# Kernel tuning notes

Measured on AMD Instinct MI355X. Metric: run time of the kernel, lower is better.

## Reference

```python
import jax, jax.numpy as jnp
import numpy as np
from jax import lax

N, C_IN, L = 32, 256, 4096
C_OUT, K, GROUPS = 256, 9, 4
C_DIM, PAD, STRIDE = 128, 4, 1


def setup_inputs() -> dict:
    key = jax.random.key(0)
    k1, k2, k3, k4, k5 = jax.random.split(key, 5)
    x = jax.random.normal(k1, (N, C_IN, L), dtype=jnp.float32)
    c = jax.random.normal(k2, (N, C_DIM), dtype=jnp.float32)
    weight = jax.random.normal(k3, (C_OUT, C_IN // GROUPS, K), dtype=jnp.float32)
    c_weight = jax.random.normal(k4, (C_OUT, C_DIM), dtype=jnp.float32)
    bias = jax.random.normal(k5, (C_OUT,), dtype=jnp.float32)
    return {"x": x, "c": c, "weight": weight, "c_weight": c_weight, "bias": bias}


def reference(x, c, weight, c_weight, bias):
    # Grouped conv1d: equivalent to the unfold+per-group matmul in the torch code.
    # dims: x (N, C_in, L), weight (C_out, C_in/groups, K) -> out (N, C_out, L_out)
    out = lax.conv_general_dilated(
        x, weight,
        window_strides=(STRIDE,),
        padding=[(PAD, PAD)],
        dimension_numbers=("NCH", "OIH", "NCH"),
        feature_group_count=GROUPS,
    )
    # Concat-path context: cat([patches, c]) @ cat([W, cW]).T == conv(x) + c @ cW.T,
    # with the context term broadcast over all temporal positions.
    ctx = jnp.einsum("nd,od->no", c, c_weight)  # (N, C_out)
    out = out + ctx[:, :, None] + bias[None, :, None]
    return out
```

## Files before the change

kernel.cpp:

```cpp
#include <hip/hip_runtime.h>
#include <hip/hip_bf16.h>

#define NB     32
#define CIN    256
#define LIN    4096
#define COUT   256
#define KW     9
#define NGRP   4
#define CDIM   128
#define CPG    64
#define LT     256
#define NROWS  264
#define RP     68
#define WF_ELEMS (4*4*9*2*64*8)

typedef __attribute__((ext_vector_type(8))) short short8;
typedef __attribute__((ext_vector_type(4))) short short4v;
typedef __attribute__((ext_vector_type(4))) float float4v;
typedef __attribute__((ext_vector_type(4))) unsigned short ushort4v;

__global__ void pack_weights(const float* __restrict__ w, __hip_bfloat16* __restrict__ wF) {
    int tid = blockIdx.x * blockDim.x + threadIdx.x;
    if (tid >= WF_ELEMS) return;
    int j    = tid & 7;
    int lane = (tid >> 3) & 63;
    int rest = tid >> 9;
    int chunk = rest & 1;  rest >>= 1;
    int k     = rest % 9;  rest /= 9;
    int co16  = rest & 3;
    int g     = rest >> 2;
    int co = g * CPG + co16 * 16 + (lane & 15);
    int ci = chunk * 32 + (lane >> 4) * 8 + j;
    wF[tid] = __float2bfloat16(w[(co * CPG + ci) * KW + k]);
}

__global__ __launch_bounds__(256) void ctx_kernel(const float* __restrict__ c,
                                                  const float* __restrict__ cw,
                                                  const float* __restrict__ bias,
                                                  float* __restrict__ ctxb) {
    int gw   = (blockIdx.x * 256 + threadIdx.x) >> 6;
    int lane = threadIdx.x & 63;
    int n  = gw >> 8;
    int co = gw & 255;
    float s = c[n * CDIM + lane]      * cw[co * CDIM + lane]
            + c[n * CDIM + 64 + lane] * cw[co * CDIM + 64 + lane];
    #pragma unroll
    for (int off = 32; off; off >>= 1) s += __shfl_down(s, off);
    if (lane == 0) ctxb[gw] = s + bias[co];
}

__global__ __launch_bounds__(256, 4) void conv_mfma(
    const float* __restrict__ x, const __hip_bfloat16* __restrict__ wF,
    const float* __restrict__ ctxb, float* __restrict__ out)
{
    __shared__ unsigned short sx[NROWS * RP];
    __shared__ float sctx[CPG];

    const int bx = blockIdx.x;
    const int t  = bx & 15;
    const int g  = (bx >> 4) & 3;
    const int n  = bx >> 6;
    const int l0 = t * LT;
    const int tid = threadIdx.x;
    const int lane = tid & 63;
    const int wv   = tid >> 6;

    if (tid < CPG) sctx[tid] = ctxb[n * COUT + g * CPG + tid];

    const float* xb = x + ((size_t)(n * CIN + g * CPG)) * LIN;

    {
        int q4  = 1 + (lane & 15);
        int cqb = 4 * wv + (lane >> 4);
        #pragma unroll
        for (int i = 0; i < 4; ++i, q4 += 16) {
            int lg = l0 - 4 + 4 * q4;
            float4v v[4];
            #pragma unroll
            for (int j = 0; j < 4; ++j)
                v[j] = *(const float4v*)(xb + (size_t)(4 * cqb + j) * LIN + lg);
            int row = 4 * q4;
            #pragma unroll
            for (int d = 0; d < 4; ++d) {
                ushort4v p;
                #pragma unroll
                for (int j = 0; j < 4; ++j)
                    p[j] = __builtin_bit_cast(unsigned short, __float2bfloat16(v[j][d]));
                *(ushort4v*)(&sx[(row + d) * RP + 4 * cqb]) = p;
            }
        }
    }
    if (tid < 32) {
        int head = (tid < 16);
        int q4 = head ? 0 : 65;
        int cq = tid & 15;
        int lg = l0 - 4 + 4 * q4;
        bool ok = head ? (t > 0) : (t < 15);
        float4v v[4];
        #pragma unroll
        for (int j = 0; j < 4; ++j)
            v[j] = ok ? *(const float4v*)(xb + (size_t)(4 * cq + j) * LIN + lg)
                      : (float4v){0.f, 0.f, 0.f, 0.f};
        int row = 4 * q4;
        #pragma unroll
        for (int d = 0; d < 4; ++d) {
            ushort4v p;
            #pragma unroll
            for (int j = 0; j < 4; ++j)
                p[j] = __builtin_bit_cast(unsigned short, __float2bfloat16(v[j][d]));
            *(ushort4v*)(&sx[(row + d) * RP + 4 * cq]) = p;
        }
    }
    __syncthreads();

    const int r  = lane & 15;
    const int q  = lane >> 4;
    const int wl = wv * 64;

    float4v acc[4][4];
    #pragma unroll
    for (int a = 0; a < 4; ++a)
        #pragma unroll
        for (int b = 0; b < 4; ++b)
            acc[a][b] = (float4v){0.f, 0.f, 0.f, 0.f};

    const short8* wFp = (const short8*)wF;

    #pragma unroll
    for (int k = 0; k < KW; ++k) {
        #pragma unroll
        for (int chunk = 0; chunk < 2; ++chunk) {
            short8 bfrag[4];
            #pragma unroll
            for (int l16 = 0; l16 < 4; ++l16) {
                int row = wl + l16 * 16 + r + k;
                int base = row * RP + chunk * 32 + q * 8;
                short4v lo = *(const short4v*)(&sx[base]);
                short4v hi = *(const short4v*)(&sx[base + 4]);
                bfrag[l16] = __builtin_shufflevector(lo, hi, 0, 1, 2, 3, 4, 5, 6, 7);
            }
            short8 afrag[4];
            #pragma unroll
            for (int co16 = 0; co16 < 4; ++co16) {
                afrag[co16] = wFp[(((g * 4 + co16) * 9 + k) * 2 + chunk) * 64 + lane];
            }
            #pragma unroll
            for (int co16 = 0; co16 < 4; ++co16)
                #pragma unroll
                for (int l16 = 0; l16 < 4; ++l16)
                    acc[co16][l16] = __builtin_amdgcn_mfma_f32_16x16x32_bf16(
                        afrag[co16], bfrag[l16], acc[co16][l16], 0, 0, 0);
        }
    }

    float* ob = out + ((size_t)(n * COUT + g * CPG)) * LIN + l0 + wl;
    #pragma unroll
    for (int co16 = 0; co16 < 4; ++co16) {
        #pragma unroll
        for (int reg = 0; reg < 4; ++reg) {
            int co_l = co16 * 16 + q * 4 + reg;
            float add = sctx[co_l];
            #pragma unroll
            for (int l16 = 0; l16 < 4; ++l16) {
                ob[(size_t)co_l * LIN + l16 * 16 + r] = acc[co16][l16][reg] + add;
            }
        }
    }
}

extern "C" void kernel_launch(void* const* d_in, const int* in_sizes, int n_in,
                              void* d_out, int out_size, void* d_ws, size_t ws_size,
                              hipStream_t stream) {
    const float* x    = (const float*)d_in[0];
    const float* c    = (const float*)d_in[1];
    const float* w    = (const float*)d_in[2];
    const float* cw   = (const float*)d_in[3];
    const float* bias = (const float*)d_in[4];
    float* out = (float*)d_out;

    __hip_bfloat16* wF = (__hip_bfloat16*)d_ws;
    float* ctxb = (float*)((char*)d_ws + (size_t)WF_ELEMS * 2);

    pack_weights<<<(WF_ELEMS + 255) / 256, 256, 0, stream>>>(w, wF);
    ctx_kernel<<<(NB * COUT * 64) / 256, 256, 0, stream>>>(c, cw, bias, ctxb);
    conv_mfma<<<NB * NGRP * (LIN / LT), 256, 0, stream>>>(x, wF, ctxb, out);
}
```

Measured before the change: 259.9 us.

## Loop each block over four L tiles with double-buffered LDS prefetch

Each block now walks four consecutive 128-wide L tiles instead of computing one 256-wide tile. While the MFMAs run on the current LDS buffer, the next tile's x data and halo are loaded into registers, then converted to bf16 and written into a second LDS buffer. The four waves are rearranged as a 2x2 split over L and output channels, so each wave holds half as many accumulators. The aim is to hide global load latency behind compute, at the cost of twice the LDS footprint and a smaller grid.

```diff
diff --git a/kernel.cpp b/kernel.cpp
--- a/kernel.cpp
+++ b/kernel.cpp
@@ -9,9 +9,11 @@
 #define NGRP   4
 #define CDIM   128
 #define CPG    64
-#define LT     256
-#define NROWS  264
+#define LT     128
+#define NROWS  136
 #define RP     68
+#define TPB    4
+#define NTILES 32
 #define WF_ELEMS (4*4*9*2*64*8)
 
 typedef __attribute__((ext_vector_type(8))) short short8;
@@ -53,15 +55,14 @@
     const float* __restrict__ x, const __hip_bfloat16* __restrict__ wF,
     const float* __restrict__ ctxb, float* __restrict__ out)
 {
-    __shared__ unsigned short sx[NROWS * RP];
+    __shared__ unsigned short sx[2][NROWS * RP];
     __shared__ float sctx[CPG];
 
     const int bx = blockIdx.x;
-    const int t  = bx & 15;
-    const int g  = (bx >> 4) & 3;
-    const int n  = bx >> 6;
-    const int l0 = t * LT;
-    const int tid = threadIdx.x;
+    const int tb = bx & 7;
+    const int g  = (bx >> 3) & 3;
+    const int n  = bx >> 5;
+    const int tid  = threadIdx.x;
     const int lane = tid & 63;
     const int wv   = tid >> 6;
 
@@ -69,102 +70,132 @@
 
     const float* xb = x + ((size_t)(n * CIN + g * CPG)) * LIN;
 
-    {
-        int q4  = 1 + (lane & 15);
-        int cqb = 4 * wv + (lane >> 4);
-        #pragma unroll
-        for (int i = 0; i < 4; ++i, q4 += 16) {
-            int lg = l0 - 4 + 4 * q4;
-            float4v v[4];
+    const int cqb = 4 * wv + (lane >> 4);
+    const int q4a = 1 + (lane & 15);
+
+    float4v mv[8];
+    float4v hv[2];
+
+    auto issue_main = [&](int l0) {
+        #pragma unroll
+        for (int i = 0; i < 2; ++i) {
+            int lg = l0 - 4 + 4 * (q4a + 16 * i);
             #pragma unroll
             for (int j = 0; j < 4; ++j)
-                v[j] = *(const float4v*)(xb + (size_t)(4 * cqb + j) * LIN + lg);
-            int row = 4 * q4;
+                mv[4 * i + j] = *(const float4v*)(xb + (size_t)(4 * cqb + j) * LIN + lg);
+        }
+    };
+    auto issue_halo = [&](int gt, int l0) {
+        if (tid < 64) {
+            int side = tid >> 5;
+            bool ok  = side ? (gt < NTILES - 1) : (gt > 0);
+            int lg   = side ? (l0 + LT) : (l0 - 4);
+            int cr   = 4 * ((tid >> 1) & 15) + 2 * (tid & 1);
+            #pragma unroll
+            for (int j = 0; j < 2; ++j)
+                hv[j] = ok ? *(const float4v*)(xb + (size_t)(cr + j) * LIN + lg)
+                           : (float4v){0.f, 0.f, 0.f, 0.f};
+        }
+    };
+    auto write_tile = [&](unsigned short* s) {
+        #pragma unroll
+        for (int i = 0; i < 2; ++i) {
+            int row0 = 4 * (q4a + 16 * i);
             #pragma unroll
             for (int d = 0; d < 4; ++d) {
                 ushort4v p;
                 #pragma unroll
                 for (int j = 0; j < 4; ++j)
-                    p[j] = __builtin_bit_cast(unsigned short, __float2bfloat16(v[j][d]));
-                *(ushort4v*)(&sx[(row + d) * RP + 4 * cqb]) = p;
-            }
-        }
-    }
-    if (tid < 32) {
-        int head = (tid < 16);
-        int q4 = head ? 0 : 65;
-        int cq = tid & 15;
-        int lg = l0 - 4 + 4 * q4;
-        bool ok = head ? (t > 0) : (t < 15);
-        float4v v[4];
-        #pragma unroll
-        for (int j = 0; j < 4; ++j)
-            v[j] = ok ? *(const float4v*)(xb + (size_t)(4 * cq + j) * LIN + lg)
-                      : (float4v){0.f, 0.f, 0.f, 0.f};
-        int row = 4 * q4;
-        #pragma unroll
-        for (int d = 0; d < 4; ++d) {
-            ushort4v p;
-            #pragma unroll
-            for (int j = 0; j < 4; ++j)
-                p[j] = __builtin_bit_cast(unsigned short, __float2bfloat16(v[j][d]));
-            *(ushort4v*)(&sx[(row + d) * RP + 4 * cq]) = p;
-        }
-    }
-    __syncthreads();
+                    p[j] = __builtin_bit_cast(unsigned short, __float2bfloat16(mv[4 * i + j][d]));
+                *(ushort4v*)(&s[(row0 + d) * RP + 4 * cqb]) = p;
+            }
+        }
+        if (tid < 64) {
+            int side = tid >> 5;
+            int row0 = side ? (NROWS - 4) : 0;
+            int off  = 4 * ((tid >> 1) & 15) + 2 * (tid & 1);
+            #pragma unroll
+            for (int d = 0; d < 4; ++d) {
+                unsigned int pp =
+                    (unsigned int)__builtin_bit_cast(unsigned short, __float2bfloat16(hv[0][d]))
+                  | ((unsigned int)__builtin_bit_cast(unsigned short, __float2bfloat16(hv[1][d])) << 16);
+                *(unsigned int*)(&s[(row0 + d) * RP + off]) = pp;
+            }
+        }
+    };
 
     const int r  = lane & 15;
     const int q  = lane >> 4;
-    const int wl = wv * 64;
-
-    float4v acc[4][4];
-    #pragma unroll
-    for (int a = 0; a < 4; ++a)
-        #pragma unroll
-        for (int b = 0; b < 4; ++b)
-            acc[a][b] = (float4v){0.f, 0.f, 0.f, 0.f};
+    const int wl = (wv >> 1) * 64;
+    const int wc = (wv & 1) * 32;
+    const int c0 = (wv & 1) * 2;
 
     const short8* wFp = (const short8*)wF;
-
-    #pragma unroll
-    for (int k = 0; k < KW; ++k) {
-        #pragma unroll
-        for (int chunk = 0; chunk < 2; ++chunk) {
-            short8 bfrag[4];
-            #pragma unroll
-            for (int l16 = 0; l16 < 4; ++l16) {
-                int row = wl + l16 * 16 + r + k;
-                int base = row * RP + chunk * 32 + q * 8;
-                short4v lo = *(const short4v*)(&sx[base]);
-                short4v hi = *(const short4v*)(&sx[base + 4]);
-                bfrag[l16] = __builtin_shufflevector(lo, hi, 0, 1, 2, 3, 4, 5, 6, 7);
-            }
-            short8 afrag[4];
-            #pragma unroll
-            for (int co16 = 0; co16 < 4; ++co16) {
-                afrag[co16] = wFp[(((g * 4 + co16) * 9 + k) * 2 + chunk) * 64 + lane];
-            }
-            #pragma unroll
-            for (int co16 = 0; co16 < 4; ++co16)
+    const int gt0 = tb * TPB;
+
+    issue_main(gt0 * LT);
+    issue_halo(gt0, gt0 * LT);
+    write_tile(sx[0]);
+    __syncthreads();
+
+    for (int it = 0; it < TPB; ++it) {
+        const int gt = gt0 + it;
+        const int l0 = gt * LT;
+
+        if (it + 1 < TPB) {
+            issue_main(l0 + LT);
+            issue_halo(gt + 1, l0 + LT);
+        }
+
+        const unsigned short* s = sx[it & 1];
+        float4v acc[2][4];
+        #pragma unroll
+        for (int a = 0; a < 2; ++a)
+            #pragma unroll
+            for (int b = 0; b < 4; ++b)
+                acc[a][b] = (float4v){0.f, 0.f, 0.f, 0.f};
+
+        #pragma unroll
+        for (int k = 0; k < KW; ++k) {
+            #pragma unroll
+            for (int chunk = 0; chunk < 2; ++chunk) {
+                short8 bfrag[4];
+                #pragma unroll
+                for (int l16 = 0; l16 < 4; ++l16) {
+                    int base = (wl + l16 * 16 + r + k) * RP + chunk * 32 + q * 8;
+                    short4v lo = *(const short4v*)(&s[base]);
+                    short4v hi = *(const short4v*)(&s[base + 4]);
+                    bfrag[l16] = __builtin_shufflevector(lo, hi, 0, 1, 2, 3, 4, 5, 6, 7);
+                }
+                short8 afrag[2];
+                #pragma unroll
+                for (int c2 = 0; c2 < 2; ++c2)
+                    afrag[c2] = wFp[(((g * 4 + c0 + c2) * 9 + k) * 2 + chunk) * 64 + lane];
+                #pragma unroll
+                for (int c2 = 0; c2 < 2; ++c2)
+                    #pragma unroll
+                    for (int l16 = 0; l16 < 4; ++l16)
+                        acc[c2][l16] = __builtin_amdgcn_mfma_f32_16x16x32_bf16(
+                            afrag[c2], bfrag[l16], acc[c2][l16], 0, 0, 0);
+            }
+        }
+
+        if (it + 1 < TPB) write_tile(sx[(it + 1) & 1]);
+
+        float* ob = out + ((size_t)(n * COUT + g * CPG)) * LIN + l0 + wl;
+        #pragma unroll
+        for (int c2 = 0; c2 < 2; ++c2) {
+            #pragma unroll
+            for (int reg = 0; reg < 4; ++reg) {
+                int co_l = wc + c2 * 16 + q * 4 + reg;
+                float add = sctx[co_l];
                 #pragma unroll
                 for (int l16 = 0; l16 < 4; ++l16)
-                    acc[co16][l16] = __builtin_amdgcn_mfma_f32_16x16x32_bf16(
-                        afrag[co16], bfrag[l16], acc[co16][l16], 0, 0, 0);
-        }
-    }
-
-    float* ob = out + ((size_t)(n * COUT + g * CPG)) * LIN + l0 + wl;
-    #pragma unroll
-    for (int co16 = 0; co16 < 4; ++co16) {
-        #pragma unroll
-        for (int reg = 0; reg < 4; ++reg) {
-            int co_l = co16 * 16 + q * 4 + reg;
-            float add = sctx[co_l];
-            #pragma unroll
-            for (int l16 = 0; l16 < 4; ++l16) {
-                ob[(size_t)co_l * LIN + l16 * 16 + r] = acc[co16][l16][reg] + add;
-            }
-        }
+                    ob[(size_t)co_l * LIN + l16 * 16 + r] = acc[c2][l16][reg] + add;
+            }
+        }
+
+        if (it + 1 < TPB) __syncthreads();
     }
 }
 
@@ -183,5 +214,5 @@
 
     pack_weights<<<(WF_ELEMS + 255) / 256, 256, 0, stream>>>(w, wF);
     ctx_kernel<<<(NB * COUT * 64) / 256, 256, 0, stream>>>(c, cw, bias, ctxb);
-    conv_mfma<<<NB * NGRP * (LIN / LT), 256, 0, stream>>>(x, wF, ctxb, out);
-}
+    conv_mfma<<<NB * NGRP * (NTILES / TPB), 256, 0, stream>>>(x, wF, ctxb, out);
+}
```

Result: slower. 382.8 us (+47.3%).
